# Kernel optimization log

Measured on AMD Instinct MI355X. Metric: run time of the kernel, lower is better.

The kernel has to match this reference:

```python
import jax, jax.numpy as jnp
import numpy as np

ADMP = 8  # admp_channel -> K = ADMP*ADMP keypoints


def setup_inputs() -> dict:
    key = jax.random.key(0)
    kA, kB = jax.random.split(key)
    B, C, H, W = 8, 512, 96, 96
    feature_A = jax.random.normal(kA, (B, C, H, W), dtype=jnp.float32)
    feature_B = jax.random.normal(kB, (B, C, H, W), dtype=jnp.float32)
    return {"feature_A": feature_A, "feature_B": feature_B}


def _keypoint_rowcol(feature_A):
    # featureSelect: sum over channels, AdaptiveMaxPool2d(ADMP) with return_indices.
    # H,W divisible by ADMP so adaptive pool == uniform non-overlapping pooling.
    B, C, H, W = feature_A.shape
    ph, pw = H // ADMP, W // ADMP
    resp = feature_A.sum(axis=1)  # [B,H,W]
    r = resp.reshape(B, ADMP, ph, ADMP, pw).transpose(0, 1, 3, 2, 4)
    r = r.reshape(B, ADMP * ADMP, ph * pw)
    loc = jnp.argmax(r, axis=-1)  # first-max, matches torch  [B,K]
    kk = jnp.arange(ADMP * ADMP)
    gi, gj = kk // ADMP, kk % ADMP
    row_A = gi[None, :] * ph + loc // pw  # [B,K]
    col_A = gj[None, :] * pw + loc % pw
    return row_A, col_A


def reference(feature_A, feature_B):
    B, C, H, W = feature_A.shape
    K = ADMP * ADMP
    row_A, col_A = _keypoint_rowcol(feature_A)
    flat_A = row_A * W + col_A  # [B,K]

    # gather descriptors: [B,K,C]
    fa = feature_A.reshape(B, C, H * W)
    desc = jnp.take_along_axis(fa, flat_A[:, None, :], axis=2).transpose(0, 2, 1)

    # squared L2 distance map via ||b||^2 - 2 a.b + ||a||^2 : [B,K,HW]
    fb = feature_B.reshape(B, C, H * W)
    fb_sq = jnp.sum(fb * fb, axis=1)            # [B,HW]
    d_sq = jnp.sum(desc * desc, axis=-1)        # [B,K]
    cross = jnp.einsum('bkc,bcn->bkn', desc, fb)  # [B,K,HW]
    dist = fb_sq[:, None, :] - 2.0 * cross + d_sq[:, :, None]

    min_idx = jnp.argmin(dist, axis=-1)  # [B,K]
    row_B = min_idx // W
    col_B = min_idx % W
    drow = -(row_B - row_A)
    dcol = -(col_B - col_A)
    off = jnp.stack([drow, dcol], axis=-1)  # [B,K,2] int

    # getTranslationalOffsetByMode: most frequent (drow,dcol) pair per batch
    eq = jnp.all(off[:, :, None, :] == off[:, None, :, :], axis=-1)  # [B,K,K]
    counts = eq.sum(axis=-1)  # [B,K]
    best = jnp.argmax(counts, axis=-1)  # first occurrence on ties, matches dict order
    out = jnp.take_along_axis(off, best[:, None, None], axis=1)[:, 0, :]  # [B,2]
    return out
```

## Files before the change

### kernel.cpp

```cpp
#include <hip/hip_runtime.h>
#include <hip/hip_bf16.h>
#include <math.h>

typedef _Float16 half8 __attribute__((ext_vector_type(8)));
typedef float f32x4 __attribute__((ext_vector_type(4)));
typedef unsigned short u16x4 __attribute__((ext_vector_type(4)));

#define B_   8
#define C_   512
#define H_   96
#define W_   96
#define HW   9216
#define K_   64
#define PH   12
#define PW   12
#define NT   96
#define CCH  32
#define NBLK 96

#define OFF_PARTIAL 0u
#define OFF_CANDV   0u
#define OFF_CANDN   294912u
#define OFF_DESCH   2359296u
#define OFF_DESCL   2883584u
#define OFF_ROWA    3407872u
#define OFF_COLA    3409920u

#define FBT_HI 0
#define FBT_LO 3072
#define DSC_HI 6144
#define DSC_LO 8192
#define BUFHW  10240

#define GLOAD_LDS16(g, l)                                                     \
    __builtin_amdgcn_global_load_lds(                                         \
        (const __attribute__((address_space(1))) unsigned int*)(g),           \
        (__attribute__((address_space(3))) unsigned int*)(l), 16, 0, 0)

__global__ __launch_bounds__(256) void k_partial(const float* __restrict__ A,
                                                 float* __restrict__ part) {
    int idx4 = blockIdx.x * 256 + threadIdx.x;
    int chunk = blockIdx.y;
    int b = idx4 / (HW / 4), hw4 = idx4 - b * (HW / 4);
    const float* p = A + ((size_t)(b * C_ + chunk * 64)) * HW + hw4 * 4;
    float4 s = make_float4(0.f, 0.f, 0.f, 0.f);
#pragma unroll
    for (int i = 0; i < 64; ++i) {
        float4 v = *(const float4*)&p[(size_t)i * HW];
        s.x += v.x; s.y += v.y; s.z += v.z; s.w += v.w;
    }
    *(float4*)&part[chunk * (B_ * HW) + b * HW + hw4 * 4] = s;
}

__global__ void k_selgather(const float* __restrict__ part, const float* __restrict__ A,
                            int* __restrict__ rowA, int* __restrict__ colA,
                            _Float16* __restrict__ descH, _Float16* __restrict__ descL) {
    int k = blockIdx.x, b = blockIdx.y, lane = threadIdx.x;
    int gi = k >> 3, gj = k & 7;
    float bv = -1e30f; int bp = 1 << 20;
    for (int p = lane; p < PH * PW; p += 64) {
        int lr = p / PW, lc = p - lr * PW;
        int hw = (gi * PH + lr) * W_ + gj * PW + lc;
        float v = 0.f;
#pragma unroll
        for (int ch = 0; ch < 8; ++ch) v += part[ch * (B_ * HW) + b * HW + hw];
        if (v > bv || (v == bv && p < bp)) { bv = v; bp = p; }
    }
    for (int m = 1; m < 64; m <<= 1) {
        float ov = __shfl_xor(bv, m);
        int   op = __shfl_xor(bp, m);
        if (ov > bv || (ov == bv && op < bp)) { bv = ov; bp = op; }
    }
    int lr = bp / PW, lc = bp - lr * PW;
    int r = gi * PH + lr, c = gj * PW + lc;
    int flat = r * W_ + c;
    if (lane == 0) { rowA[b * K_ + k] = r; colA[b * K_ + k] = c; }
#pragma unroll
    for (int i = 0; i < 8; ++i) {
        int cc = i * 64 + lane;
        float v = A[((size_t)(b * C_ + cc)) * HW + flat];
        _Float16 h = (_Float16)v;
        _Float16 lo = (_Float16)((v - (float)h) * 2048.f);
        size_t o = ((size_t)(b * K_ + k)) * C_ + cc;
        descH[o] = h; descL[o] = lo;
    }
}

__global__ __launch_bounds__(256, 3) void k_main(const float* __restrict__ FB,
                                                 const _Float16* __restrict__ descH,
                                                 const _Float16* __restrict__ descL,
                                                 float* __restrict__ candV,
                                                 int* __restrict__ candN) {
    __shared__ __attribute__((aligned(16))) unsigned short smem_us[2 * BUFHW];
    int b = blockIdx.y, nb = blockIdx.x * NT;
    int tid = threadIdx.x;
    int l = tid & 63;
    int w = tid >> 6;
    const size_t baseB = (size_t)b * C_ * HW + nb;

    const int so = tid % 12;
    const int scb = tid / 12;
    const int st_nt = so >> 1, st_nn0 = (so & 1) * 8;

    const _Float16* dH = descH + ((size_t)(b * K_) + w * 16 + (l >> 2)) * C_ + (l & 3) * 8;
    const _Float16* dL = descL + ((size_t)(b * K_) + w * 16 + (l >> 2)) * C_ + (l & 3) * 8;

    f32x4 accH[6], accX[6];
#pragma unroll
    for (int nt = 0; nt < 6; ++nt) {
        accH[nt] = (f32x4){0.f, 0.f, 0.f, 0.f};
        accX[nt] = (f32x4){0.f, 0.f, 0.f, 0.f};
    }
    float sq[8];
#pragma unroll
    for (int j = 0; j < 8; ++j) sq[j] = 0.f;

    float4 r0a, r0b, r1a, r1b;

#define LOADFB(c0)                                                            \
    do {                                                                      \
        if (tid < 192) {                                                      \
            const float* p0 = &FB[baseB + (size_t)((c0) + scb) * HW + so * 8];      \
            const float* p1 = &FB[baseB + (size_t)((c0) + scb + 16) * HW + so * 8]; \
            r0a = *(const float4*)p0; r0b = *(const float4*)(p0 + 4);         \
            r1a = *(const float4*)p1; r1b = *(const float4*)(p1 + 4);         \
        }                                                                     \
    } while (0)

#define CVT8(va, vb, hofs)                                                    \
    do {                                                                      \
        float vv[8] = {va.x, va.y, va.z, va.w, vb.x, vb.y, vb.z, vb.w};       \
        half8 h8, l8;                                                         \
        _Pragma("unroll")                                                     \
        for (int j = 0; j < 8; ++j) {                                         \
            float v = vv[j];                                                  \
            _Float16 hh = (_Float16)v;                                        \
            l8[j] = (_Float16)((v - (float)hh) * 2048.f);                     \
            h8[j] = hh;                                                       \
            sq[j] = fmaf(v, v, sq[j]);                                        \
        }                                                                     \
        *(half8*)&smem_us[(hofs)] = h8;                                       \
        *(half8*)&smem_us[(hofs) + FBT_LO] = l8;                              \
    } while (0)

#define WRITEFB(bufhw)                                                        \
    do {                                                                      \
        if (tid < 192) {                                                      \
            int c = scb;                                                      \
            int off0 = (bufhw) + FBT_HI + st_nt * 512 + ((c >> 2) & 1) * 256  \
                       + (c >> 3) * 64 + (c & 3) * 16 + st_nn0;               \
            CVT8(r0a, r0b, off0);                                             \
            c = scb + 16;                                                     \
            int off1 = (bufhw) + FBT_HI + st_nt * 512 + ((c >> 2) & 1) * 256  \
                       + (c >> 3) * 64 + (c & 3) * 16 + st_nn0;               \
            CVT8(r1a, r1b, off1);                                             \
        }                                                                     \
    } while (0)

#define STAGEDESC(bufhw, c0)                                                  \
    do {                                                                      \
        GLOAD_LDS16(dH + (c0), &smem_us[(bufhw) + DSC_HI + w * 512]);         \
        GLOAD_LDS16(dL + (c0), &smem_us[(bufhw) + DSC_LO + w * 512]);         \
    } while (0)

    LOADFB(0);
    STAGEDESC(0, 0);
    WRITEFB(0);
    __syncthreads();

    const unsigned lds0 = (unsigned)(size_t)&smem_us[0];
    const unsigned trlane = (unsigned)l * 8u;

    for (int t = 0; t < 16; ++t) {
        const int cur = (t & 1) ? BUFHW : 0;
        const int nxt = BUFHW - cur;
        if (t < 15) { LOADFB((t + 1) * CCH); STAGEDESC(nxt, (t + 1) * CCH); }

        half8 aH = *(half8*)&smem_us[cur + DSC_HI + (w * 16 + (l & 15)) * 32 + (l >> 4) * 8];
        half8 aL = *(half8*)&smem_us[cur + DSC_LO + (w * 16 + (l & 15)) * 32 + (l >> 4) * 8];
        const unsigned trb = lds0 + (unsigned)(cur + FBT_HI) * 2u + trlane;
#pragma unroll
        for (int nt = 0; nt < 6; ++nt) {
            u16x4 h0, h1, q0, q1;
            unsigned a0 = trb + (unsigned)nt * 1024u;
            asm volatile("ds_read_b64_tr_b16 %0, %1" : "=v"(h0) : "v"(a0));
            asm volatile("ds_read_b64_tr_b16 %0, %1 offset:512" : "=v"(h1) : "v"(a0));
            asm volatile("ds_read_b64_tr_b16 %0, %1 offset:6144" : "=v"(q0) : "v"(a0));
            asm volatile("ds_read_b64_tr_b16 %0, %1 offset:6656" : "=v"(q1) : "v"(a0));
            asm volatile("s_waitcnt lgkmcnt(0)" ::: "memory");
            __builtin_amdgcn_sched_barrier(0);
            union { u16x4 q[2]; half8 h; } uH, uL;
            uH.q[0] = h0; uH.q[1] = h1;
            uL.q[0] = q0; uL.q[1] = q1;
            accH[nt] = __builtin_amdgcn_mfma_f32_16x16x32_f16(aH, uH.h, accH[nt], 0, 0, 0);
            accX[nt] = __builtin_amdgcn_mfma_f32_16x16x32_f16(aH, uL.h, accX[nt], 0, 0, 0);
            accX[nt] = __builtin_amdgcn_mfma_f32_16x16x32_f16(aL, uH.h, accX[nt], 0, 0, 0);
        }
        if (t < 15) WRITEFB(nxt);
        __syncthreads();
    }

    float* fscr = (float*)&smem_us[0];
    if (tid < 192) {
        *(float4*)&fscr[scb * 96 + so * 8]     = make_float4(sq[0], sq[1], sq[2], sq[3]);
        *(float4*)&fscr[scb * 96 + so * 8 + 4] = make_float4(sq[4], sq[5], sq[6], sq[7]);
    }
    __syncthreads();
    if (tid < 96) {
        float s = 0.f;
#pragma unroll
        for (int g = 0; g < 16; ++g) s += fscr[g * 96 + tid];
        fscr[1536 + tid] = s;
    }
    __syncthreads();

    const float inv2048 = 1.f / 2048.f;
#pragma unroll
    for (int r = 0; r < 4; ++r) {
        float bv = 1e30f; int bn = 1 << 28;
#pragma unroll
        for (int nt = 0; nt < 6; ++nt) {
            float cross = accH[nt][r] + accX[nt][r] * inv2048;
            float d = fscr[1536 + nt * 16 + (l & 15)] - 2.f * cross;
            int n = nb + nt * 16 + (l & 15);
            if (d < bv) { bv = d; bn = n; }
        }
#pragma unroll
        for (int m = 1; m < 16; m <<= 1) {
            float ov = __shfl_xor(bv, m);
            int   on = __shfl_xor(bn, m);
            if (ov < bv || (ov == bv && on < bn)) { bv = ov; bn = on; }
        }
        if ((l & 15) == 0) {
            int k = w * 16 + (l >> 4) * 4 + r;
            candV[(b * K_ + k) * NBLK + blockIdx.x] = bv;
            candN[(b * K_ + k) * NBLK + blockIdx.x] = bn;
        }
    }
#undef LOADFB
#undef CVT8
#undef WRITEFB
#undef STAGEDESC
}

__global__ void k_redmode(const float* __restrict__ candV, const int* __restrict__ candN,
                          const int* __restrict__ rowA, const int* __restrict__ colA,
                          int* __restrict__ out) {
    __shared__ int r_s[64], c_s[64];
    int b = blockIdx.x, k = threadIdx.x;
    int base = (b * K_ + k) * NBLK;
    float bv = 1e30f; int bn = 1 << 28;
    for (int j = 0; j < NBLK; ++j) {
        float ov = candV[base + j]; int on = candN[base + j];
        if (ov < bv || (ov == bv && on < bn)) { bv = ov; bn = on; }
    }
    int rB = bn / W_, cB = bn - rB * W_;
    r_s[k] = rowA[b * K_ + k] - rB;
    c_s[k] = colA[b * K_ + k] - cB;
    __syncthreads();
    int mr = r_s[k], mc = c_s[k], cnt = 0;
#pragma unroll
    for (int j = 0; j < 64; ++j) cnt += (r_s[j] == mr && c_s[j] == mc) ? 1 : 0;
    int bk = k, bc = cnt;
    for (int m = 1; m < 64; m <<= 1) {
        int oc = __shfl_xor(bc, m);
        int ok = __shfl_xor(bk, m);
        if (oc > bc || (oc == bc && ok < bk)) { bc = oc; bk = ok; }
    }
    if (k == 0) { out[b * 2] = r_s[bk]; out[b * 2 + 1] = c_s[bk]; }
}

extern "C" void kernel_launch(void* const* d_in, const int* in_sizes, int n_in,
                              void* d_out, int out_size, void* d_ws, size_t ws_size,
                              hipStream_t stream) {
    const float* A  = (const float*)d_in[0];
    const float* FB = (const float*)d_in[1];
    char* ws = (char*)d_ws;
    float*     part  = (float*)(ws + OFF_PARTIAL);
    _Float16*  descH = (_Float16*)(ws + OFF_DESCH);
    _Float16*  descL = (_Float16*)(ws + OFF_DESCL);
    int*       rowA  = (int*)(ws + OFF_ROWA);
    int*       colA  = (int*)(ws + OFF_COLA);
    float*     candV = (float*)(ws + OFF_CANDV);
    int*       candN = (int*)(ws + OFF_CANDN);
    int*       out   = (int*)d_out;

    k_partial<<<dim3((B_ * HW) / 1024, 8), 256, 0, stream>>>(A, part);
    k_selgather<<<dim3(K_, B_), 64, 0, stream>>>(part, A, rowA, colA, descH, descL);
    k_main<<<dim3(NBLK, B_), 256, 0, stream>>>(FB, descH, descL, candV, candN);
    k_redmode<<<dim3(B_), 64, 0, stream>>>(candV, candN, rowA, colA, out);
}
```

Before: 93.58 us.

## Software-pipeline LDS transpose reads with MFMAs and pad descriptor staging

Replaces the per-tile wait-all on the LDS transpose reads with a double-buffered schedule. The next tile's four ds_read_b64_tr_b16 are issued before waiting with lgkmcnt(4), so LDS latency overlaps the MFMAs. Descriptor staging moves from global_load_lds into register loads followed by padded LDS writes (row stride 40), which avoids bank conflicts on the A-fragment reads. FP32-to-FP16 hi/lo splitting now uses packed round-toward-zero conversion (cvt_pkrtz). That changes rounding of the hi part but keeps the hi+lo compensation, and it adds register pressure and a larger LDS footprint.

After: 93.89 us. About the same (+0.3%).

```diff
diff --git a/kernel.cpp b/kernel.cpp
--- a/kernel.cpp
+++ b/kernel.cpp
@@ -3,8 +3,10 @@
 #include <math.h>
 
 typedef _Float16 half8 __attribute__((ext_vector_type(8)));
+typedef __fp16 fp16x2 __attribute__((ext_vector_type(2)));
 typedef float f32x4 __attribute__((ext_vector_type(4)));
 typedef unsigned short u16x4 __attribute__((ext_vector_type(4)));
+typedef unsigned short u16x8 __attribute__((ext_vector_type(8)));
 
 #define B_   8
 #define C_   512
@@ -29,13 +31,8 @@
 #define FBT_HI 0
 #define FBT_LO 3072
 #define DSC_HI 6144
-#define DSC_LO 8192
-#define BUFHW  10240
-
-#define GLOAD_LDS16(g, l)                                                     \
-    __builtin_amdgcn_global_load_lds(                                         \
-        (const __attribute__((address_space(1))) unsigned int*)(g),           \
-        (__attribute__((address_space(3))) unsigned int*)(l), 16, 0, 0)
+#define DSC_LO 8704
+#define BUFHW  11264
 
 __global__ __launch_bounds__(256) void k_partial(const float* __restrict__ A,
                                                  float* __restrict__ part) {
@@ -101,9 +98,7 @@
     const int so = tid % 12;
     const int scb = tid / 12;
     const int st_nt = so >> 1, st_nn0 = (so & 1) * 8;
-
-    const _Float16* dH = descH + ((size_t)(b * K_) + w * 16 + (l >> 2)) * C_ + (l & 3) * 8;
-    const _Float16* dL = descL + ((size_t)(b * K_) + w * 16 + (l >> 2)) * C_ + (l & 3) * 8;
+    const int dk = tid >> 2, dco = tid & 3;
 
     f32x4 accH[6], accX[6];
 #pragma unroll
@@ -116,6 +111,7 @@
     for (int j = 0; j < 8; ++j) sq[j] = 0.f;
 
     float4 r0a, r0b, r1a, r1b;
+    u16x8 rdH, rdL;
 
 #define LOADFB(c0)                                                            \
     do {                                                                      \
@@ -127,20 +123,30 @@
         }                                                                     \
     } while (0)
 
+#define LOADDESC(c0)                                                          \
+    do {                                                                      \
+        size_t o = ((size_t)(b * K_) + dk) * C_ + (c0) + dco * 8;             \
+        rdH = *(const u16x8*)&descH[o];                                       \
+        rdL = *(const u16x8*)&descL[o];                                       \
+    } while (0)
+
 #define CVT8(va, vb, hofs)                                                    \
     do {                                                                      \
+        union { fp16x2 p[4]; half8 h; } hh, ll;                               \
         float vv[8] = {va.x, va.y, va.z, va.w, vb.x, vb.y, vb.z, vb.w};       \
-        half8 h8, l8;                                                         \
         _Pragma("unroll")                                                     \
-        for (int j = 0; j < 8; ++j) {                                         \
-            float v = vv[j];                                                  \
-            _Float16 hh = (_Float16)v;                                        \
-            l8[j] = (_Float16)((v - (float)hh) * 2048.f);                     \
-            h8[j] = hh;                                                       \
-            sq[j] = fmaf(v, v, sq[j]);                                        \
+        for (int j = 0; j < 4; ++j) {                                         \
+            float a = vv[2 * j], bq = vv[2 * j + 1];                          \
+            fp16x2 hp = __builtin_amdgcn_cvt_pkrtz(a, bq);                    \
+            float ha = (float)hp[0], hb = (float)hp[1];                       \
+            fp16x2 lp = __builtin_amdgcn_cvt_pkrtz((a - ha) * 2048.f,         \
+                                                   (bq - hb) * 2048.f);       \
+            hh.p[j] = hp; ll.p[j] = lp;                                       \
+            sq[2 * j]     = fmaf(a, a, sq[2 * j]);                            \
+            sq[2 * j + 1] = fmaf(bq, bq, sq[2 * j + 1]);                      \
         }                                                                     \
-        *(half8*)&smem_us[(hofs)] = h8;                                       \
-        *(half8*)&smem_us[(hofs) + FBT_LO] = l8;                              \
+        *(half8*)&smem_us[(hofs)] = hh.h;                                     \
+        *(half8*)&smem_us[(hofs) + FBT_LO] = ll.h;                            \
     } while (0)
 
 #define WRITEFB(bufhw)                                                        \
@@ -157,46 +163,72 @@
         }                                                                     \
     } while (0)
 
-#define STAGEDESC(bufhw, c0)                                                  \
-    do {                                                                      \
-        GLOAD_LDS16(dH + (c0), &smem_us[(bufhw) + DSC_HI + w * 512]);         \
-        GLOAD_LDS16(dL + (c0), &smem_us[(bufhw) + DSC_LO + w * 512]);         \
+#define WRITEDESC(bufhw)                                                      \
+    do {                                                                      \
+        *(u16x8*)&smem_us[(bufhw) + DSC_HI + dk * 40 + dco * 8] = rdH;        \
+        *(u16x8*)&smem_us[(bufhw) + DSC_LO + dk * 40 + dco * 8] = rdL;        \
     } while (0)
 
     LOADFB(0);
-    STAGEDESC(0, 0);
+    LOADDESC(0);
     WRITEFB(0);
+    WRITEDESC(0);
     __syncthreads();
 
     const unsigned lds0 = (unsigned)(size_t)&smem_us[0];
-    const unsigned trlane = (unsigned)l * 8u;
+
+#define TRQ(d0, d1, d2, d3, addr)                                             \
+    asm volatile("ds_read_b64_tr_b16 %0, %1"             : "=v"(d0) : "v"(addr)); \
+    asm volatile("ds_read_b64_tr_b16 %0, %1 offset:512"  : "=v"(d1) : "v"(addr)); \
+    asm volatile("ds_read_b64_tr_b16 %0, %1 offset:6144" : "=v"(d2) : "v"(addr)); \
+    asm volatile("ds_read_b64_tr_b16 %0, %1 offset:6656" : "=v"(d3) : "v"(addr));
+
+#define WAIT4 asm volatile("s_waitcnt lgkmcnt(4)" ::: "memory");              \
+              __builtin_amdgcn_sched_barrier(0);
+#define WAIT0 asm volatile("s_waitcnt lgkmcnt(0)" ::: "memory");              \
+              __builtin_amdgcn_sched_barrier(0);
+
+#define MFMA3(nt, h0_, h1_, l0_, l1_)                                         \
+    do {                                                                      \
+        union { u16x4 q[2]; half8 h; } bh, bl;                                \
+        bh.q[0] = h0_; bh.q[1] = h1_; bl.q[0] = l0_; bl.q[1] = l1_;           \
+        accH[nt] = __builtin_amdgcn_mfma_f32_16x16x32_f16(aHu.h, bh.h, accH[nt], 0, 0, 0); \
+        accX[nt] = __builtin_amdgcn_mfma_f32_16x16x32_f16(aHu.h, bl.h, accX[nt], 0, 0, 0); \
+        accX[nt] = __builtin_amdgcn_mfma_f32_16x16x32_f16(aLu.h, bh.h, accX[nt], 0, 0, 0); \
+    } while (0)
 
     for (int t = 0; t < 16; ++t) {
         const int cur = (t & 1) ? BUFHW : 0;
         const int nxt = BUFHW - cur;
-        if (t < 15) { LOADFB((t + 1) * CCH); STAGEDESC(nxt, (t + 1) * CCH); }
-
-        half8 aH = *(half8*)&smem_us[cur + DSC_HI + (w * 16 + (l & 15)) * 32 + (l >> 4) * 8];
-        half8 aL = *(half8*)&smem_us[cur + DSC_LO + (w * 16 + (l & 15)) * 32 + (l >> 4) * 8];
-        const unsigned trb = lds0 + (unsigned)(cur + FBT_HI) * 2u + trlane;
-#pragma unroll
-        for (int nt = 0; nt < 6; ++nt) {
-            u16x4 h0, h1, q0, q1;
-            unsigned a0 = trb + (unsigned)nt * 1024u;
-            asm volatile("ds_read_b64_tr_b16 %0, %1" : "=v"(h0) : "v"(a0));
-            asm volatile("ds_read_b64_tr_b16 %0, %1 offset:512" : "=v"(h1) : "v"(a0));
-            asm volatile("ds_read_b64_tr_b16 %0, %1 offset:6144" : "=v"(q0) : "v"(a0));
-            asm volatile("ds_read_b64_tr_b16 %0, %1 offset:6656" : "=v"(q1) : "v"(a0));
-            asm volatile("s_waitcnt lgkmcnt(0)" ::: "memory");
-            __builtin_amdgcn_sched_barrier(0);
-            union { u16x4 q[2]; half8 h; } uH, uL;
-            uH.q[0] = h0; uH.q[1] = h1;
-            uL.q[0] = q0; uL.q[1] = q1;
-            accH[nt] = __builtin_amdgcn_mfma_f32_16x16x32_f16(aH, uH.h, accH[nt], 0, 0, 0);
-            accX[nt] = __builtin_amdgcn_mfma_f32_16x16x32_f16(aH, uL.h, accX[nt], 0, 0, 0);
-            accX[nt] = __builtin_amdgcn_mfma_f32_16x16x32_f16(aL, uH.h, accX[nt], 0, 0, 0);
-        }
-        if (t < 15) WRITEFB(nxt);
+        if (t < 15) { LOADFB((t + 1) * CCH); LOADDESC((t + 1) * CCH); }
+
+        union { u16x8 u; half8 h; } aHu, aLu;
+        const unsigned abase = lds0 +
+            (unsigned)(cur + DSC_HI + (w * 16 + (l & 15)) * 40 + (l >> 4) * 8) * 2u;
+        asm volatile("ds_read_b128 %0, %1"             : "=v"(aHu.u) : "v"(abase));
+        asm volatile("ds_read_b128 %0, %1 offset:5120" : "=v"(aLu.u) : "v"(abase));
+        const unsigned trb = lds0 + (unsigned)cur * 2u + (unsigned)l * 8u;
+        u16x4 xh0, xh1, xl0, xl1, yh0, yh1, yl0, yl1;
+        TRQ(xh0, xh1, xl0, xl1, trb);
+        TRQ(yh0, yh1, yl0, yl1, trb + 1024u);
+        WAIT4;
+        MFMA3(0, xh0, xh1, xl0, xl1);
+        TRQ(xh0, xh1, xl0, xl1, trb + 2048u);
+        WAIT4;
+        MFMA3(1, yh0, yh1, yl0, yl1);
+        TRQ(yh0, yh1, yl0, yl1, trb + 3072u);
+        WAIT4;
+        MFMA3(2, xh0, xh1, xl0, xl1);
+        TRQ(xh0, xh1, xl0, xl1, trb + 4096u);
+        WAIT4;
+        MFMA3(3, yh0, yh1, yl0, yl1);
+        TRQ(yh0, yh1, yl0, yl1, trb + 5120u);
+        WAIT4;
+        MFMA3(4, xh0, xh1, xl0, xl1);
+        WAIT0;
+        MFMA3(5, yh0, yh1, yl0, yl1);
+
+        if (t < 15) { WRITEFB(nxt); WRITEDESC(nxt); }
         __syncthreads();
     }
 
@@ -238,9 +270,14 @@
         }
     }
 #undef LOADFB
+#undef LOADDESC
 #undef CVT8
 #undef WRITEFB
-#undef STAGEDESC
+#undef WRITEDESC
+#undef TRQ
+#undef WAIT4
+#undef WAIT0
+#undef MFMA3
 }
 
 __global__ void k_redmode(const float* __restrict__ candV, const int* __restrict__ candN,
```
